# Kernel optimization log

Hardware: AMD Instinct MI355X
Metric: run time of the kernel (lower is better)

## Reference

```python
import jax, jax.numpy as jnp
import numpy as np

B = 262144   # number of (group, item) prediction pairs
M = 16       # max members per group (ragged -> padded)
NU = 100000  # num_users
NI = 50000   # num_items
D = 32       # embedding_dim (hardcoded via torch.zeros([32]))


def setup_inputs() -> dict:
    key = jax.random.key(0)
    ks = jax.random.split(key, 9)
    item_inputs = jax.random.randint(ks[0], (B,), 0, NI)
    member_ids = jax.random.randint(ks[1], (B, M), 0, NU)
    lengths = jax.random.randint(ks[2], (B, 1), 1, M + 1)
    member_mask = jnp.arange(M)[None, :] < lengths  # [B, M] bool, variable group sizes
    user_table = jax.random.normal(ks[3], (NU, D), jnp.float32) * 0.1  # xavier-ish
    item_table = jax.random.normal(ks[4], (NI, D), jnp.float32) * 0.1
    W_bil = jax.random.normal(ks[5], (D, D), jnp.float32)  # nn.Bilinear(D, D, 1) weight[0]
    b_bil = jax.random.normal(ks[6], (1,), jnp.float32) * 0.05
    W1 = jax.random.normal(ks[7], (8, 3 * D), jnp.float32) * 0.05  # Linear(96, 8)
    b1 = jnp.zeros((8,), jnp.float32)
    W2 = jax.random.normal(ks[8], (1, 8), jnp.float32) * 0.05  # Linear(8, 1)
    b2 = jnp.zeros((1,), jnp.float32)
    return {
        "item_inputs": item_inputs, "member_ids": member_ids, "member_mask": member_mask,
        "user_table": user_table, "item_table": item_table,
        "W_bil": W_bil, "b_bil": b_bil, "W1": W1, "b1": b1, "W2": W2, "b2": b2,
    }


def reference(item_inputs, member_ids, member_mask, user_table, item_table,
              W_bil, b_bil, W1, b1, W2, b2):
    item_e = item_table[item_inputs]          # [B, D] gather
    mem_e = user_table[member_ids]            # [B, M, D] gather
    # bilinear attention score per member: m^T W i + b (softmax in original is computed then discarded)
    scores = jnp.einsum('bmd,de,be->bm', mem_e, W_bil, item_e) + b_bil[0]
    w = scores * member_mask.astype(scores.dtype)  # zero out padded members (ragged groups)
    final_user = jnp.einsum('bm,bmd->bd', w, mem_e)  # unnormalized weighted sum of members
    new_embeds = jnp.concatenate([final_user * item_e, final_user, item_e], axis=-1)  # [B, 3D]
    h = jax.nn.relu(new_embeds @ W1.T + b1)
    y = jax.nn.sigmoid(h @ W2.T + b2)          # [B, 1]
    return y
```

## Files before the change

### kernel.cpp

```cpp
#include <hip/hip_runtime.h>
#include <math.h>

#define DD 32
#define MM 16

__device__ __forceinline__ void load8f4(const float* __restrict__ p, float* r) {
    const float4* q = (const float4*)p;
#pragma unroll
    for (int i = 0; i < 8; ++i) {
        float4 v = q[i];
        r[4*i+0] = v.x; r[4*i+1] = v.y; r[4*i+2] = v.z; r[4*i+3] = v.w;
    }
}

__global__ void precompute_item(const float* __restrict__ item_table,
                                const float* __restrict__ W_bil,
                                const float* __restrict__ W1,
                                float* __restrict__ tbl, int NI) {
    int i = blockIdx.x * blockDim.x + threadIdx.x;
    if (i >= NI) return;
    float it[DD];
    load8f4(item_table + (size_t)i * DD, it);
    float* o = tbl + (size_t)i * 40;
#pragma unroll 4
    for (int d = 0; d < DD; ++d) {
        float s = 0.f;
#pragma unroll
        for (int e = 0; e < DD; ++e) s = fmaf(W_bil[d * DD + e], it[e], s);
        o[d] = s;
    }
#pragma unroll
    for (int j = 0; j < 8; ++j) {
        float s = 0.f;
#pragma unroll
        for (int d = 0; d < DD; ++d) s = fmaf(W1[j * 96 + 64 + d], it[d], s);
        o[32 + j] = s;
    }
}

template <bool USE_TBL>
__global__ void bilinear_main(const int* __restrict__ item_inputs,
                              const int* __restrict__ member_ids,
                              const unsigned char* __restrict__ member_mask,
                              const float* __restrict__ user_table,
                              const float* __restrict__ item_table,
                              const float* __restrict__ tbl,
                              const float* __restrict__ W_bil,
                              const float* __restrict__ b_bil,
                              const float* __restrict__ W1,
                              const float* __restrict__ b1,
                              const float* __restrict__ W2,
                              const float* __restrict__ b2,
                              float* __restrict__ out, int Btot) {
    int b = blockIdx.x * blockDim.x + threadIdx.x;
    if (b >= Btot) return;

    int item = item_inputs[b];

    uint4 mv = *(const uint4*)(member_mask + (size_t)b * MM);
    int len = __popc(mv.x & 0x01010101u) + __popc(mv.y & 0x01010101u) +
              __popc(mv.z & 0x01010101u) + __popc(mv.w & 0x01010101u);

    int ids[MM];
    {
        const int4* mp = (const int4*)(member_ids + (size_t)b * MM);
#pragma unroll
        for (int q = 0; q < 4; ++q) {
            int4 v = mp[q];
            ids[4*q+0] = v.x; ids[4*q+1] = v.y; ids[4*q+2] = v.z; ids[4*q+3] = v.w;
        }
    }

    float t[DD];
    float cj[8];
    if (USE_TBL) {
        const float* tb = tbl + (size_t)item * 40;
        load8f4(tb, t);
        float4 c0 = *(const float4*)(tb + 32);
        float4 c1 = *(const float4*)(tb + 36);
        cj[0] = c0.x; cj[1] = c0.y; cj[2] = c0.z; cj[3] = c0.w;
        cj[4] = c1.x; cj[5] = c1.y; cj[6] = c1.z; cj[7] = c1.w;
    } else {
        float it0[DD];
        load8f4(item_table + (size_t)item * DD, it0);
#pragma unroll 4
        for (int d = 0; d < DD; ++d) {
            float s = 0.f;
#pragma unroll
            for (int e = 0; e < DD; ++e) s = fmaf(W_bil[d * DD + e], it0[e], s);
            t[d] = s;
        }
#pragma unroll
        for (int j = 0; j < 8; ++j) {
            float s = 0.f;
#pragma unroll
            for (int d = 0; d < DD; ++d) s = fmaf(W1[j * 96 + 64 + d], it0[d], s);
            cj[j] = s;
        }
    }

    float bb = b_bil[0];
    float fin[DD];
#pragma unroll
    for (int d = 0; d < DD; ++d) fin[d] = 0.f;

    for (int m = 0; m < len; ++m) {
        float me[DD];
        load8f4(user_table + (size_t)ids[m] * DD, me);
        float s = bb;
#pragma unroll
        for (int d = 0; d < DD; ++d) s = fmaf(me[d], t[d], s);
#pragma unroll
        for (int d = 0; d < DD; ++d) fin[d] = fmaf(s, me[d], fin[d]);
    }

    float it[DD];
    load8f4(item_table + (size_t)item * DD, it);

    float h[8];
#pragma unroll
    for (int j = 0; j < 8; ++j) h[j] = cj[j] + b1[j];
#pragma unroll
    for (int d = 0; d < DD; ++d) {
        float f = fin[d];
        float p = f * it[d];
#pragma unroll
        for (int j = 0; j < 8; ++j) {
            h[j] = fmaf(W1[j * 96 + d], p, h[j]);
            h[j] = fmaf(W1[j * 96 + 32 + d], f, h[j]);
        }
    }
    float z = b2[0];
#pragma unroll
    for (int j = 0; j < 8; ++j) {
        float hv = h[j] > 0.f ? h[j] : 0.f;
        z = fmaf(W2[j], hv, z);
    }
    out[b] = 1.f / (1.f + __expf(-z));
}

extern "C" void kernel_launch(void* const* d_in, const int* in_sizes, int n_in,
                              void* d_out, int out_size, void* d_ws, size_t ws_size,
                              hipStream_t stream) {
    const int*           item_inputs = (const int*)d_in[0];
    const int*           member_ids  = (const int*)d_in[1];
    const unsigned char* member_mask = (const unsigned char*)d_in[2];
    const float*         user_table  = (const float*)d_in[3];
    const float*         item_table  = (const float*)d_in[4];
    const float*         W_bil       = (const float*)d_in[5];
    const float*         b_bil       = (const float*)d_in[6];
    const float*         W1          = (const float*)d_in[7];
    const float*         b1          = (const float*)d_in[8];
    const float*         W2          = (const float*)d_in[9];
    const float*         b2          = (const float*)d_in[10];
    float* out = (float*)d_out;

    int Btot = in_sizes[0];
    int NI   = in_sizes[4] / DD;

    bool use_tbl = ws_size >= (size_t)NI * 40 * sizeof(float);
    int blk = 256;
    if (use_tbl) {
        float* tbl = (float*)d_ws;
        precompute_item<<<(NI + blk - 1) / blk, blk, 0, stream>>>(item_table, W_bil, W1, tbl, NI);
        bilinear_main<true><<<(Btot + blk - 1) / blk, blk, 0, stream>>>(
            item_inputs, member_ids, member_mask, user_table, item_table, tbl,
            W_bil, b_bil, W1, b1, W2, b2, out, Btot);
    } else {
        bilinear_main<false><<<(Btot + blk - 1) / blk, blk, 0, stream>>>(
            item_inputs, member_ids, member_mask, user_table, item_table, nullptr,
            W_bil, b_bil, W1, b1, W2, b2, out, Btot);
    }
}
```

Baseline: 144.4 us.

## Split each batch row across 8 lanes with shuffle reductions

Measured after the change: 162.9 us. 12.8% more time.

```diff
diff --git a/kernel.cpp b/kernel.cpp
--- a/kernel.cpp
+++ b/kernel.cpp
@@ -4,56 +4,73 @@
 #define DD 32
 #define MM 16
 
-__device__ __forceinline__ void load8f4(const float* __restrict__ p, float* r) {
-    const float4* q = (const float4*)p;
-#pragma unroll
-    for (int i = 0; i < 8; ++i) {
-        float4 v = q[i];
-        r[4*i+0] = v.x; r[4*i+1] = v.y; r[4*i+2] = v.z; r[4*i+3] = v.w;
-    }
-}
-
-__global__ void precompute_item(const float* __restrict__ item_table,
-                                const float* __restrict__ W_bil,
-                                const float* __restrict__ W1,
-                                float* __restrict__ tbl, int NI) {
-    int i = blockIdx.x * blockDim.x + threadIdx.x;
+__device__ __forceinline__ float rsum8(float v) {
+    v += __shfl_xor(v, 1);
+    v += __shfl_xor(v, 2);
+    v += __shfl_xor(v, 4);
+    return v;
+}
+
+__global__ void precompute_item8(const float* __restrict__ item_table,
+                                 const float* __restrict__ W_bil,
+                                 const float* __restrict__ W1,
+                                 float* __restrict__ tbl, int NI) {
+    int gid = blockIdx.x * blockDim.x + threadIdx.x;
+    int i = gid >> 3, l = gid & 7;
     if (i >= NI) return;
-    float it[DD];
-    load8f4(item_table + (size_t)i * DD, it);
+    float4 it[8];
+    const float4* q = (const float4*)(item_table + (size_t)i * DD);
+#pragma unroll
+    for (int k = 0; k < 8; ++k) it[k] = q[k];
+    float tt[4];
+#pragma unroll
+    for (int r = 0; r < 4; ++r) {
+        const float4* w = (const float4*)(W_bil + (size_t)(4 * l + r) * DD);
+        float s = 0.f;
+#pragma unroll
+        for (int k = 0; k < 8; ++k) {
+            float4 wv = w[k];
+            s = fmaf(wv.x, it[k].x, s);
+            s = fmaf(wv.y, it[k].y, s);
+            s = fmaf(wv.z, it[k].z, s);
+            s = fmaf(wv.w, it[k].w, s);
+        }
+        tt[r] = s;
+    }
+    float cj = 0.f;
+    const float4* w1 = (const float4*)(W1 + l * 96 + 64);
+#pragma unroll
+    for (int k = 0; k < 8; ++k) {
+        float4 wv = w1[k];
+        cj = fmaf(wv.x, it[k].x, cj);
+        cj = fmaf(wv.y, it[k].y, cj);
+        cj = fmaf(wv.z, it[k].z, cj);
+        cj = fmaf(wv.w, it[k].w, cj);
+    }
     float* o = tbl + (size_t)i * 40;
-#pragma unroll 4
-    for (int d = 0; d < DD; ++d) {
-        float s = 0.f;
-#pragma unroll
-        for (int e = 0; e < DD; ++e) s = fmaf(W_bil[d * DD + e], it[e], s);
-        o[d] = s;
-    }
-#pragma unroll
-    for (int j = 0; j < 8; ++j) {
-        float s = 0.f;
-#pragma unroll
-        for (int d = 0; d < DD; ++d) s = fmaf(W1[j * 96 + 64 + d], it[d], s);
-        o[32 + j] = s;
-    }
+    *(float4*)(o + 4 * l) = make_float4(tt[0], tt[1], tt[2], tt[3]);
+    o[32 + l] = cj;
 }
 
 template <bool USE_TBL>
-__global__ void bilinear_main(const int* __restrict__ item_inputs,
-                              const int* __restrict__ member_ids,
-                              const unsigned char* __restrict__ member_mask,
-                              const float* __restrict__ user_table,
-                              const float* __restrict__ item_table,
-                              const float* __restrict__ tbl,
-                              const float* __restrict__ W_bil,
-                              const float* __restrict__ b_bil,
-                              const float* __restrict__ W1,
-                              const float* __restrict__ b1,
-                              const float* __restrict__ W2,
-                              const float* __restrict__ b2,
-                              float* __restrict__ out, int Btot) {
-    int b = blockIdx.x * blockDim.x + threadIdx.x;
+__global__ void bilinear_main8(const int* __restrict__ item_inputs,
+                               const int* __restrict__ member_ids,
+                               const unsigned char* __restrict__ member_mask,
+                               const float* __restrict__ user_table,
+                               const float* __restrict__ item_table,
+                               const float* __restrict__ tbl,
+                               const float* __restrict__ W_bil,
+                               const float* __restrict__ b_bil,
+                               const float* __restrict__ W1,
+                               const float* __restrict__ b1,
+                               const float* __restrict__ W2,
+                               const float* __restrict__ b2,
+                               float* __restrict__ out, int Btot) {
+    int gid = blockIdx.x * blockDim.x + threadIdx.x;
+    int b = gid >> 3;
+    int l = threadIdx.x & 7;
     if (b >= Btot) return;
+    int laneBase = (threadIdx.x & 63) & 56;
 
     int item = item_inputs[b];
 
@@ -61,82 +78,106 @@
     int len = __popc(mv.x & 0x01010101u) + __popc(mv.y & 0x01010101u) +
               __popc(mv.z & 0x01010101u) + __popc(mv.w & 0x01010101u);
 
-    int ids[MM];
-    {
-        const int4* mp = (const int4*)(member_ids + (size_t)b * MM);
-#pragma unroll
-        for (int q = 0; q < 4; ++q) {
-            int4 v = mp[q];
-            ids[4*q+0] = v.x; ids[4*q+1] = v.y; ids[4*q+2] = v.z; ids[4*q+3] = v.w;
-        }
-    }
-
-    float t[DD];
-    float cj[8];
+    int2 id2 = ((const int2*)(member_ids + (size_t)b * MM))[l];
+
+    float4 t4;
+    float  cjl;
     if (USE_TBL) {
         const float* tb = tbl + (size_t)item * 40;
-        load8f4(tb, t);
-        float4 c0 = *(const float4*)(tb + 32);
-        float4 c1 = *(const float4*)(tb + 36);
-        cj[0] = c0.x; cj[1] = c0.y; cj[2] = c0.z; cj[3] = c0.w;
-        cj[4] = c1.x; cj[5] = c1.y; cj[6] = c1.z; cj[7] = c1.w;
+        t4  = *(const float4*)(tb + 4 * l);
+        cjl = tb[32 + l];
     } else {
-        float it0[DD];
-        load8f4(item_table + (size_t)item * DD, it0);
-#pragma unroll 4
-        for (int d = 0; d < DD; ++d) {
+        float4 it[8];
+        const float4* q = (const float4*)(item_table + (size_t)item * DD);
+#pragma unroll
+        for (int k = 0; k < 8; ++k) it[k] = q[k];
+        float tt[4];
+#pragma unroll
+        for (int r = 0; r < 4; ++r) {
+            const float4* w = (const float4*)(W_bil + (size_t)(4 * l + r) * DD);
             float s = 0.f;
 #pragma unroll
-            for (int e = 0; e < DD; ++e) s = fmaf(W_bil[d * DD + e], it0[e], s);
-            t[d] = s;
+            for (int k = 0; k < 8; ++k) {
+                float4 wv = w[k];
+                s = fmaf(wv.x, it[k].x, s); s = fmaf(wv.y, it[k].y, s);
+                s = fmaf(wv.z, it[k].z, s); s = fmaf(wv.w, it[k].w, s);
+            }
+            tt[r] = s;
         }
-#pragma unroll
-        for (int j = 0; j < 8; ++j) {
-            float s = 0.f;
-#pragma unroll
-            for (int d = 0; d < DD; ++d) s = fmaf(W1[j * 96 + 64 + d], it0[d], s);
-            cj[j] = s;
+        t4 = make_float4(tt[0], tt[1], tt[2], tt[3]);
+        cjl = 0.f;
+        const float4* w1 = (const float4*)(W1 + l * 96 + 64);
+#pragma unroll
+        for (int k = 0; k < 8; ++k) {
+            float4 wv = w1[k];
+            cjl = fmaf(wv.x, it[k].x, cjl); cjl = fmaf(wv.y, it[k].y, cjl);
+            cjl = fmaf(wv.z, it[k].z, cjl); cjl = fmaf(wv.w, it[k].w, cjl);
         }
     }
 
     float bb = b_bil[0];
-    float fin[DD];
-#pragma unroll
-    for (int d = 0; d < DD; ++d) fin[d] = 0.f;
-
-    for (int m = 0; m < len; ++m) {
-        float me[DD];
-        load8f4(user_table + (size_t)ids[m] * DD, me);
-        float s = bb;
-#pragma unroll
-        for (int d = 0; d < DD; ++d) s = fmaf(me[d], t[d], s);
-#pragma unroll
-        for (int d = 0; d < DD; ++d) fin[d] = fmaf(s, me[d], fin[d]);
-    }
-
-    float it[DD];
-    load8f4(item_table + (size_t)item * DD, it);
-
-    float h[8];
-#pragma unroll
-    for (int j = 0; j < 8; ++j) h[j] = cj[j] + b1[j];
-#pragma unroll
-    for (int d = 0; d < DD; ++d) {
-        float f = fin[d];
-        float p = f * it[d];
-#pragma unroll
-        for (int j = 0; j < 8; ++j) {
-            h[j] = fmaf(W1[j * 96 + d], p, h[j]);
-            h[j] = fmaf(W1[j * 96 + 32 + d], f, h[j]);
-        }
-    }
+    float4 fin = make_float4(0.f, 0.f, 0.f, 0.f);
+
+    for (int c = 0; c < 4; ++c) {
+        int m0 = 4 * c;
+        if (m0 >= len) break;
+        int sA = laneBase | (2 * c);
+        int sB = laneBase | (2 * c + 1);
+        int ida = __shfl(id2.x, sA);
+        int idb = __shfl(id2.y, sA);
+        int idc = __shfl(id2.x, sB);
+        int idd = __shfl(id2.y, sB);
+        float4 ma = *(const float4*)(user_table + (size_t)ida * DD + 4 * l);
+        float4 mb = *(const float4*)(user_table + (size_t)idb * DD + 4 * l);
+        float4 mc = *(const float4*)(user_table + (size_t)idc * DD + 4 * l);
+        float4 md = *(const float4*)(user_table + (size_t)idd * DD + 4 * l);
+
+        float pa = ma.x * t4.x; pa = fmaf(ma.y, t4.y, pa); pa = fmaf(ma.z, t4.z, pa); pa = fmaf(ma.w, t4.w, pa);
+        float pb = mb.x * t4.x; pb = fmaf(mb.y, t4.y, pb); pb = fmaf(mb.z, t4.z, pb); pb = fmaf(mb.w, t4.w, pb);
+        float pc = mc.x * t4.x; pc = fmaf(mc.y, t4.y, pc); pc = fmaf(mc.z, t4.z, pc); pc = fmaf(mc.w, t4.w, pc);
+        float pd = md.x * t4.x; pd = fmaf(md.y, t4.y, pd); pd = fmaf(md.z, t4.z, pd); pd = fmaf(md.w, t4.w, pd);
+        pa = rsum8(pa); pb = rsum8(pb); pc = rsum8(pc); pd = rsum8(pd);
+        float sa = (m0 + 0 < len) ? (pa + bb) : 0.f;
+        float sb = (m0 + 1 < len) ? (pb + bb) : 0.f;
+        float sc = (m0 + 2 < len) ? (pc + bb) : 0.f;
+        float sd = (m0 + 3 < len) ? (pd + bb) : 0.f;
+        fin.x = fmaf(sa, ma.x, fin.x); fin.y = fmaf(sa, ma.y, fin.y);
+        fin.z = fmaf(sa, ma.z, fin.z); fin.w = fmaf(sa, ma.w, fin.w);
+        fin.x = fmaf(sb, mb.x, fin.x); fin.y = fmaf(sb, mb.y, fin.y);
+        fin.z = fmaf(sb, mb.z, fin.z); fin.w = fmaf(sb, mb.w, fin.w);
+        fin.x = fmaf(sc, mc.x, fin.x); fin.y = fmaf(sc, mc.y, fin.y);
+        fin.z = fmaf(sc, mc.z, fin.z); fin.w = fmaf(sc, mc.w, fin.w);
+        fin.x = fmaf(sd, md.x, fin.x); fin.y = fmaf(sd, md.y, fin.y);
+        fin.z = fmaf(sd, md.z, fin.z); fin.w = fmaf(sd, md.w, fin.w);
+    }
+
+    float4 iv = *(const float4*)(item_table + (size_t)item * DD + 4 * l);
+    float4 p4 = make_float4(fin.x * iv.x, fin.y * iv.y, fin.z * iv.z, fin.w * iv.w);
+
+    float part[8];
+#pragma unroll
+    for (int j = 0; j < 8; ++j) {
+        const float* w = W1 + j * 96;
+        float4 wa = *(const float4*)(w + 4 * l);
+        float4 wb = *(const float4*)(w + 32 + 4 * l);
+        float s = wa.x * p4.x;
+        s = fmaf(wa.y, p4.y, s); s = fmaf(wa.z, p4.z, s); s = fmaf(wa.w, p4.w, s);
+        s = fmaf(wb.x, fin.x, s); s = fmaf(wb.y, fin.y, s);
+        s = fmaf(wb.z, fin.z, s); s = fmaf(wb.w, fin.w, s);
+        part[j] = s;
+    }
+    part[l] += cjl + b1[l];
+
+#pragma unroll
+    for (int j = 0; j < 8; ++j) part[j] = rsum8(part[j]);
+
     float z = b2[0];
 #pragma unroll
     for (int j = 0; j < 8; ++j) {
-        float hv = h[j] > 0.f ? h[j] : 0.f;
-        z = fmaf(W2[j], hv, z);
-    }
-    out[b] = 1.f / (1.f + __expf(-z));
+        float h = part[j] > 0.f ? part[j] : 0.f;
+        z = fmaf(W2[j], h, z);
+    }
+    if (l == 0) out[b] = 1.f / (1.f + __expf(-z));
 }
 
 extern "C" void kernel_launch(void* const* d_in, const int* in_sizes, int n_in,
@@ -159,15 +200,17 @@
     int NI   = in_sizes[4] / DD;
 
     bool use_tbl = ws_size >= (size_t)NI * 40 * sizeof(float);
-    int blk = 256;
+    const int blk = 256;
+    int grid_main = (int)(((size_t)Btot * 8 + blk - 1) / blk);
     if (use_tbl) {
         float* tbl = (float*)d_ws;
-        precompute_item<<<(NI + blk - 1) / blk, blk, 0, stream>>>(item_table, W_bil, W1, tbl, NI);
-        bilinear_main<true><<<(Btot + blk - 1) / blk, blk, 0, stream>>>(
+        int grid_pre = (int)(((size_t)NI * 8 + blk - 1) / blk);
+        precompute_item8<<<grid_pre, blk, 0, stream>>>(item_table, W_bil, W1, tbl, NI);
+        bilinear_main8<true><<<grid_main, blk, 0, stream>>>(
             item_inputs, member_ids, member_mask, user_table, item_table, tbl,
             W_bil, b_bil, W1, b1, W2, b2, out, Btot);
     } else {
-        bilinear_main<false><<<(Btot + blk - 1) / blk, blk, 0, stream>>>(
+        bilinear_main8<false><<<grid_main, blk, 0, stream>>>(
             item_inputs, member_ids, member_mask, user_table, item_table, nullptr,
             W_bil, b_bil, W1, b1, W2, b2, out, Btot);
     }
```

## Split item precompute across 8 lanes and unroll member gathers in pairs

Applied to the files above, without the earlier changes.

Result: slower. 162.7 us (+12.7%).

```diff
diff --git a/kernel.cpp b/kernel.cpp
--- a/kernel.cpp
+++ b/kernel.cpp
@@ -13,38 +13,166 @@
     }
 }
 
-__global__ void precompute_item(const float* __restrict__ item_table,
-                                const float* __restrict__ W_bil,
-                                const float* __restrict__ W1,
-                                float* __restrict__ tbl, int NI) {
-    int i = blockIdx.x * blockDim.x + threadIdx.x;
+__device__ __forceinline__ int mask_len(const unsigned char* __restrict__ mp) {
+    uint4 mv = *(const uint4*)mp;
+    return __popc(mv.x & 0x01010101u) + __popc(mv.y & 0x01010101u) +
+           __popc(mv.z & 0x01010101u) + __popc(mv.w & 0x01010101u);
+}
+
+__device__ __forceinline__ void acc_pair(const float* __restrict__ user_table,
+                                         int idA, int idB, const float* __restrict__ t,
+                                         float bb, float* __restrict__ fin) {
+    float meA[DD], meB[DD];
+    load8f4(user_table + (size_t)idA * DD, meA);
+    load8f4(user_table + (size_t)idB * DD, meB);
+    float sA = bb, sB = bb;
+#pragma unroll
+    for (int d = 0; d < DD; ++d) sA = fmaf(meA[d], t[d], sA);
+#pragma unroll
+    for (int d = 0; d < DD; ++d) sB = fmaf(meB[d], t[d], sB);
+#pragma unroll
+    for (int d = 0; d < DD; ++d) fin[d] = fmaf(sA, meA[d], fin[d]);
+#pragma unroll
+    for (int d = 0; d < DD; ++d) fin[d] = fmaf(sB, meB[d], fin[d]);
+}
+
+__device__ __forceinline__ void acc_one(const float* __restrict__ user_table,
+                                        int idA, const float* __restrict__ t,
+                                        float bb, float* __restrict__ fin) {
+    float meA[DD];
+    load8f4(user_table + (size_t)idA * DD, meA);
+    float sA = bb;
+#pragma unroll
+    for (int d = 0; d < DD; ++d) sA = fmaf(meA[d], t[d], sA);
+#pragma unroll
+    for (int d = 0; d < DD; ++d) fin[d] = fmaf(sA, meA[d], fin[d]);
+}
+
+__device__ __forceinline__ float epilogue(const float* __restrict__ fin,
+                                          const float* __restrict__ it,
+                                          const float4 c0, const float4 c1,
+                                          const float* __restrict__ W1,
+                                          const float* __restrict__ b1,
+                                          const float* __restrict__ W2,
+                                          const float* __restrict__ b2) {
+    float h[8] = {c0.x, c0.y, c0.z, c0.w, c1.x, c1.y, c1.z, c1.w};
+#pragma unroll
+    for (int j = 0; j < 8; ++j) h[j] += b1[j];
+#pragma unroll
+    for (int d = 0; d < DD; ++d) {
+        float f = fin[d];
+        float p = f * it[d];
+#pragma unroll
+        for (int j = 0; j < 8; ++j) {
+            h[j] = fmaf(W1[j * 96 + d], p, h[j]);
+            h[j] = fmaf(W1[j * 96 + 32 + d], f, h[j]);
+        }
+    }
+    float z = b2[0];
+#pragma unroll
+    for (int j = 0; j < 8; ++j) {
+        float hv = h[j] > 0.f ? h[j] : 0.f;
+        z = fmaf(W2[j], hv, z);
+    }
+    return 1.f / (1.f + __expf(-z));
+}
+
+__global__ void precompute_item8(const float* __restrict__ item_table,
+                                 const float* __restrict__ W_bil,
+                                 const float* __restrict__ W1,
+                                 float* __restrict__ tbl, int NI) {
+    int gid = blockIdx.x * blockDim.x + threadIdx.x;
+    int i = gid >> 3, l = gid & 7;
     if (i >= NI) return;
+    float4 it[8];
+    const float4* q = (const float4*)(item_table + (size_t)i * DD);
+#pragma unroll
+    for (int k = 0; k < 8; ++k) it[k] = q[k];
+    float tt[4];
+#pragma unroll
+    for (int r = 0; r < 4; ++r) {
+        const float4* w = (const float4*)(W_bil + (size_t)(4 * l + r) * DD);
+        float s = 0.f;
+#pragma unroll
+        for (int k = 0; k < 8; ++k) {
+            float4 wv = w[k];
+            s = fmaf(wv.x, it[k].x, s); s = fmaf(wv.y, it[k].y, s);
+            s = fmaf(wv.z, it[k].z, s); s = fmaf(wv.w, it[k].w, s);
+        }
+        tt[r] = s;
+    }
+    float cj = 0.f;
+    const float4* w1 = (const float4*)(W1 + l * 96 + 64);
+#pragma unroll
+    for (int k = 0; k < 8; ++k) {
+        float4 wv = w1[k];
+        cj = fmaf(wv.x, it[k].x, cj); cj = fmaf(wv.y, it[k].y, cj);
+        cj = fmaf(wv.z, it[k].z, cj); cj = fmaf(wv.w, it[k].w, cj);
+    }
+    float* o = tbl + (size_t)i * 40;
+    *(float4*)(o + 4 * l) = make_float4(tt[0], tt[1], tt[2], tt[3]);
+    o[32 + l] = cj;
+}
+
+__global__ __launch_bounds__(256)
+void bilinear_tbl(const int* __restrict__ item_inputs,
+                  const int* __restrict__ member_ids,
+                  const unsigned char* __restrict__ member_mask,
+                  const float* __restrict__ user_table,
+                  const float* __restrict__ item_table,
+                  const float* __restrict__ tbl,
+                  const float* __restrict__ b_bil,
+                  const float* __restrict__ W1,
+                  const float* __restrict__ b1,
+                  const float* __restrict__ W2,
+                  const float* __restrict__ b2,
+                  float* __restrict__ out, int Btot) {
+    int b = blockIdx.x * blockDim.x + threadIdx.x;
+    if (b >= Btot) return;
+    int item = item_inputs[b];
+    int len = mask_len(member_mask + (size_t)b * MM);
+
+    const int4* idp = (const int4*)(member_ids + (size_t)b * MM);
+    int4 iv0 = idp[0], iv1 = idp[1], iv2 = idp[2], iv3 = idp[3];
+
+    const float* tb = tbl + (size_t)item * 40;
+    float t[DD];
+    load8f4(tb, t);
+    float bb = b_bil[0];
+
+    float fin[DD];
+#pragma unroll
+    for (int d = 0; d < DD; ++d) fin[d] = 0.f;
+
+    if (len >= 2) acc_pair(user_table, iv0.x, iv0.y, t, bb, fin);
+    else          acc_one (user_table, iv0.x, t, bb, fin);
+    if (len >= 4)       acc_pair(user_table, iv0.z, iv0.w, t, bb, fin);
+    else if (len == 3)  acc_one (user_table, iv0.z, t, bb, fin);
+    if (len >= 6)       acc_pair(user_table, iv1.x, iv1.y, t, bb, fin);
+    else if (len == 5)  acc_one (user_table, iv1.x, t, bb, fin);
+    if (len >= 8)       acc_pair(user_table, iv1.z, iv1.w, t, bb, fin);
+    else if (len == 7)  acc_one (user_table, iv1.z, t, bb, fin);
+    if (len >= 10)      acc_pair(user_table, iv2.x, iv2.y, t, bb, fin);
+    else if (len == 9)  acc_one (user_table, iv2.x, t, bb, fin);
+    if (len >= 12)      acc_pair(user_table, iv2.z, iv2.w, t, bb, fin);
+    else if (len == 11) acc_one (user_table, iv2.z, t, bb, fin);
+    if (len >= 14)      acc_pair(user_table, iv3.x, iv3.y, t, bb, fin);
+    else if (len == 13) acc_one (user_table, iv3.x, t, bb, fin);
+    if (len >= 16)      acc_pair(user_table, iv3.z, iv3.w, t, bb, fin);
+    else if (len == 15) acc_one (user_table, iv3.z, t, bb, fin);
+
     float it[DD];
-    load8f4(item_table + (size_t)i * DD, it);
-    float* o = tbl + (size_t)i * 40;
-#pragma unroll 4
-    for (int d = 0; d < DD; ++d) {
-        float s = 0.f;
-#pragma unroll
-        for (int e = 0; e < DD; ++e) s = fmaf(W_bil[d * DD + e], it[e], s);
-        o[d] = s;
-    }
-#pragma unroll
-    for (int j = 0; j < 8; ++j) {
-        float s = 0.f;
-#pragma unroll
-        for (int d = 0; d < DD; ++d) s = fmaf(W1[j * 96 + 64 + d], it[d], s);
-        o[32 + j] = s;
-    }
-}
-
-template <bool USE_TBL>
-__global__ void bilinear_main(const int* __restrict__ item_inputs,
+    load8f4(item_table + (size_t)item * DD, it);
+    float4 c0 = *(const float4*)(tb + 32);
+    float4 c1 = *(const float4*)(tb + 36);
+    out[b] = epilogue(fin, it, c0, c1, W1, b1, W2, b2);
+}
+
+__global__ void bilinear_flat(const int* __restrict__ item_inputs,
                               const int* __restrict__ member_ids,
                               const unsigned char* __restrict__ member_mask,
                               const float* __restrict__ user_table,
                               const float* __restrict__ item_table,
-                              const float* __restrict__ tbl,
                               const float* __restrict__ W_bil,
                               const float* __restrict__ b_bil,
                               const float* __restrict__ W1,
@@ -54,89 +182,45 @@
                               float* __restrict__ out, int Btot) {
     int b = blockIdx.x * blockDim.x + threadIdx.x;
     if (b >= Btot) return;
-
     int item = item_inputs[b];
-
-    uint4 mv = *(const uint4*)(member_mask + (size_t)b * MM);
-    int len = __popc(mv.x & 0x01010101u) + __popc(mv.y & 0x01010101u) +
-              __popc(mv.z & 0x01010101u) + __popc(mv.w & 0x01010101u);
-
-    int ids[MM];
-    {
-        const int4* mp = (const int4*)(member_ids + (size_t)b * MM);
-#pragma unroll
-        for (int q = 0; q < 4; ++q) {
-            int4 v = mp[q];
-            ids[4*q+0] = v.x; ids[4*q+1] = v.y; ids[4*q+2] = v.z; ids[4*q+3] = v.w;
-        }
-    }
-
+    int len = mask_len(member_mask + (size_t)b * MM);
+    float it0[DD];
+    load8f4(item_table + (size_t)item * DD, it0);
     float t[DD];
+#pragma unroll 4
+    for (int d = 0; d < DD; ++d) {
+        float s = 0.f;
+#pragma unroll
+        for (int e = 0; e < DD; ++e) s = fmaf(W_bil[d * DD + e], it0[e], s);
+        t[d] = s;
+    }
     float cj[8];
-    if (USE_TBL) {
-        const float* tb = tbl + (size_t)item * 40;
-        load8f4(tb, t);
-        float4 c0 = *(const float4*)(tb + 32);
-        float4 c1 = *(const float4*)(tb + 36);
-        cj[0] = c0.x; cj[1] = c0.y; cj[2] = c0.z; cj[3] = c0.w;
-        cj[4] = c1.x; cj[5] = c1.y; cj[6] = c1.z; cj[7] = c1.w;
-    } else {
-        float it0[DD];
-        load8f4(item_table + (size_t)item * DD, it0);
-#pragma unroll 4
-        for (int d = 0; d < DD; ++d) {
-            float s = 0.f;
-#pragma unroll
-            for (int e = 0; e < DD; ++e) s = fmaf(W_bil[d * DD + e], it0[e], s);
-            t[d] = s;
-        }
-#pragma unroll
-        for (int j = 0; j < 8; ++j) {
-            float s = 0.f;
-#pragma unroll
-            for (int d = 0; d < DD; ++d) s = fmaf(W1[j * 96 + 64 + d], it0[d], s);
-            cj[j] = s;
-        }
-    }
-
+#pragma unroll
+    for (int j = 0; j < 8; ++j) {
+        float s = 0.f;
+#pragma unroll
+        for (int d = 0; d < DD; ++d) s = fmaf(W1[j * 96 + 64 + d], it0[d], s);
+        cj[j] = s;
+    }
+    const int4* idp = (const int4*)(member_ids + (size_t)b * MM);
     float bb = b_bil[0];
     float fin[DD];
 #pragma unroll
     for (int d = 0; d < DD; ++d) fin[d] = 0.f;
-
-    for (int m = 0; m < len; ++m) {
-        float me[DD];
-        load8f4(user_table + (size_t)ids[m] * DD, me);
-        float s = bb;
-#pragma unroll
-        for (int d = 0; d < DD; ++d) s = fmaf(me[d], t[d], s);
-#pragma unroll
-        for (int d = 0; d < DD; ++d) fin[d] = fmaf(s, me[d], fin[d]);
-    }
-
-    float it[DD];
-    load8f4(item_table + (size_t)item * DD, it);
-
-    float h[8];
-#pragma unroll
-    for (int j = 0; j < 8; ++j) h[j] = cj[j] + b1[j];
-#pragma unroll
-    for (int d = 0; d < DD; ++d) {
-        float f = fin[d];
-        float p = f * it[d];
-#pragma unroll
-        for (int j = 0; j < 8; ++j) {
-            h[j] = fmaf(W1[j * 96 + d], p, h[j]);
-            h[j] = fmaf(W1[j * 96 + 32 + d], f, h[j]);
-        }
-    }
-    float z = b2[0];
-#pragma unroll
-    for (int j = 0; j < 8; ++j) {
-        float hv = h[j] > 0.f ? h[j] : 0.f;
-        z = fmaf(W2[j], hv, z);
-    }
-    out[b] = 1.f / (1.f + __expf(-z));
+#pragma unroll 1
+    for (int c = 0; c < 4; ++c) {
+        int m0 = 4 * c;
+        if (m0 >= len) break;
+        int4 iv = idp[c];
+        int rem = len - m0;
+        if (rem >= 2) acc_pair(user_table, iv.x, iv.y, t, bb, fin);
+        else          acc_one(user_table, iv.x, t, bb, fin);
+        if (rem >= 4)      acc_pair(user_table, iv.z, iv.w, t, bb, fin);
+        else if (rem == 3) acc_one(user_table, iv.z, t, bb, fin);
+    }
+    float4 c0 = make_float4(cj[0], cj[1], cj[2], cj[3]);
+    float4 c1 = make_float4(cj[4], cj[5], cj[6], cj[7]);
+    out[b] = epilogue(fin, it0, c0, c1, W1, b1, W2, b2);
 }
 
 extern "C" void kernel_launch(void* const* d_in, const int* in_sizes, int n_in,
@@ -158,17 +242,18 @@
     int Btot = in_sizes[0];
     int NI   = in_sizes[4] / DD;
 
-    bool use_tbl = ws_size >= (size_t)NI * 40 * sizeof(float);
-    int blk = 256;
-    if (use_tbl) {
+    size_t tbl_bytes = (size_t)NI * 40 * sizeof(float);
+    const int blk = 256;
+    if (ws_size >= tbl_bytes) {
         float* tbl = (float*)d_ws;
-        precompute_item<<<(NI + blk - 1) / blk, blk, 0, stream>>>(item_table, W_bil, W1, tbl, NI);
-        bilinear_main<true><<<(Btot + blk - 1) / blk, blk, 0, stream>>>(
+        int grid_pre = (int)(((size_t)NI * 8 + blk - 1) / blk);
+        precompute_item8<<<grid_pre, blk, 0, stream>>>(item_table, W_bil, W1, tbl, NI);
+        bilinear_tbl<<<(Btot + blk - 1) / blk, blk, 0, stream>>>(
             item_inputs, member_ids, member_mask, user_table, item_table, tbl,
+            b_bil, W1, b1, W2, b2, out, Btot);
+    } else {
+        bilinear_flat<<<(Btot + blk - 1) / blk, blk, 0, stream>>>(
+            item_inputs, member_ids, member_mask, user_table, item_table,
             W_bil, b_bil, W1, b1, W2, b2, out, Btot);
-    } else {
-        bilinear_main<false><<<(Btot + blk - 1) / blk, blk, 0, stream>>>(
-            item_inputs, member_ids, member_mask, user_table, item_table, nullptr,
-            W_bil, b_bil, W1, b1, W2, b2, out, Btot);
-    }
-}
+    }
+}
```
